# Performance work log

Hardware: AMD Instinct MI355X
Metric: run time of the kernel (lower is better)

Reference implementation:

```python
import jax, jax.numpy as jnp
import numpy as np

B, S, HID = 2, 2048, 4096
NH, NKV, HD = 32, 8, 128
SLIDING_WINDOW = 1024
ROPE_THETA = 10000.0


def setup_inputs() -> dict:
    key = jax.random.key(0)
    ks = jax.random.split(key, 6)
    hidden_states = jax.random.normal(ks[0], (B, S, HID), dtype=jnp.float32)
    attention_mask = jnp.ones((B, S), dtype=jnp.int32)
    position_ids = jnp.broadcast_to(jnp.arange(S, dtype=jnp.int32)[None, :], (B, S))
    sc = 1.0 / np.sqrt(HID)
    q_w = jax.random.normal(ks[1], (HID, NH * HD), dtype=jnp.float32) * sc
    k_w = jax.random.normal(ks[2], (HID, NKV * HD), dtype=jnp.float32) * sc
    v_w = jax.random.normal(ks[3], (HID, NKV * HD), dtype=jnp.float32) * sc
    o_w = jax.random.normal(ks[4], (NH * HD, HID), dtype=jnp.float32) * sc
    return {"hidden_states": hidden_states, "attention_mask": attention_mask,
            "position_ids": position_ids, "q_w": q_w, "k_w": k_w, "v_w": v_w, "o_w": o_w}


def _rotate_half(x):
    return jnp.concatenate((-x[..., x.shape[-1] // 2:], x[..., : x.shape[-1] // 2]), axis=-1)


def _rope_sincos(position_ids):
    # inv_freq over even dims of head_dim; emb = concat(freqs, freqs)
    inv_freq = 1.0 / ROPE_THETA ** (jnp.arange(0, HD, 2, dtype=jnp.float32) / HD)
    freqs = position_ids.astype(jnp.float32)[..., None] * inv_freq  # [B,S,HD/2]
    emb = jnp.concatenate((freqs, freqs), axis=-1)                  # [B,S,HD]
    # broadcast over heads axis: [B,S,1,HD]
    return jnp.sin(emb)[:, :, None, :], jnp.cos(emb)[:, :, None, :]


def reference(hidden_states, attention_mask, position_ids, q_w, k_w, v_w, o_w):
    b, q_len, _ = hidden_states.shape
    n_rep = NH // NKV

    q = (hidden_states @ q_w).reshape(b, q_len, NH, HD)
    k = (hidden_states @ k_w).reshape(b, q_len, NKV, HD)
    v = (hidden_states @ v_w).reshape(b, q_len, NKV, HD)

    sin_pos, cos_pos = _rope_sincos(position_ids)
    q = q * cos_pos + _rotate_half(q) * sin_pos
    k = k * cos_pos + _rotate_half(k) * sin_pos

    # GQA: repeat kv heads (repeat_interleave along head axis)
    k = jnp.repeat(k, n_rep, axis=2)  # [B,S,NH,HD]
    v = jnp.repeat(v, n_rep, axis=2)

    # sliding-window causal mask: j <= i and j >= i - sliding_window
    i = jnp.arange(q_len)[:, None]
    j = jnp.arange(q_len)[None, :]
    band = (j <= i) & (j >= i - SLIDING_WINDOW)           # [Q,K]
    mask = band[None, None] & (attention_mask[:, None, None, :] > 0)  # [B,1,Q,K]

    bias = jnp.where(mask, 0.0, jnp.finfo(jnp.float32).min)

    scale = 1.0 / jnp.sqrt(jnp.asarray(HD, dtype=jnp.float32))
    scores = jnp.einsum('bqhd,bkhd->bhqk', q, k) * scale + bias
    attn_weights = jax.nn.softmax(scores, axis=-1)
    attn_out = jnp.einsum('bhqk,bkhd->bqhd', attn_weights, v)
    attn_out = attn_out.reshape(b, q_len, HID)
    return attn_out @ o_w
```

## Files before the change

kernel.cpp:

```cpp
#include <hip/hip_runtime.h>
#include <stdint.h>
#include <stddef.h>

typedef __bf16 bf16x8 __attribute__((ext_vector_type(8)));
typedef short short8 __attribute__((ext_vector_type(8)));
typedef float floatx4 __attribute__((ext_vector_type(4)));
typedef unsigned short ushort4v __attribute__((ext_vector_type(4)));

__device__ __forceinline__ unsigned short f2bf(float f){
  unsigned int u = __float_as_uint(f);
  u += 0x7fffu + ((u >> 16) & 1u);
  return (unsigned short)(u >> 16);
}
__device__ __forceinline__ float bf2f(unsigned short s){
  return __uint_as_float(((unsigned int)s) << 16);
}
__device__ __forceinline__ void gl2lds16(const void* g, void* l){
  __builtin_amdgcn_global_load_lds((const __attribute__((address_space(1))) void*)g,
                                   (__attribute__((address_space(3))) void*)l, 16, 0, 0);
}

__global__ __launch_bounds__(256) void conv_f32_bf16(const float* __restrict__ in,
                                                     unsigned short* __restrict__ out){
  int t = blockIdx.x * 256 + threadIdx.x;
  floatx4 v = *(const floatx4*)(in + (size_t)t * 4);
  ushort4v o;
#pragma unroll
  for (int j = 0; j < 4; ++j) o[j] = f2bf(v[j]);
  *(ushort4v*)(out + (size_t)t * 4) = o;
}

__global__ __launch_bounds__(256) void transpose_cvt(const float* __restrict__ in,
                                                     unsigned short* __restrict__ out,
                                                     int Kd, int Nd){
  __shared__ __align__(16) unsigned short tile[64 * 80];
  int n0 = blockIdx.x * 64, k0 = blockIdx.y * 64;
  int t = threadIdx.x;
#pragma unroll
  for (int it = 0; it < 2; ++it){
    int rr = (t >> 3) + it * 32;
    int cc = t & 7;
    const float* src = in + (size_t)(k0 + rr) * Nd + n0 + cc * 8;
    floatx4 a = *(const floatx4*)src;
    floatx4 b = *(const floatx4*)(src + 4);
    short8 s;
#pragma unroll
    for (int j = 0; j < 4; ++j){ s[j] = (short)f2bf(a[j]); s[j + 4] = (short)f2bf(b[j]); }
    *(short8*)&tile[rr * 80 + cc * 8] = s;
  }
  __syncthreads();
#pragma unroll
  for (int it = 0; it < 2; ++it){
    int nr = (t >> 3) + it * 32;
    int kc = t & 7;
    short8 v;
#pragma unroll
    for (int j = 0; j < 8; ++j) v[j] = (short)tile[(kc * 8 + j) * 80 + nr];
    *(short8*)(out + (size_t)(n0 + nr) * Kd + k0 + kc * 8) = v;
  }
}

__global__ __launch_bounds__(256, 2) void gemm_bt(
    const unsigned short* __restrict__ A,
    const unsigned short* __restrict__ Wq,
    const unsigned short* __restrict__ Wk,
    const unsigned short* __restrict__ Wv,
    unsigned short* __restrict__ oQ,
    unsigned short* __restrict__ oK,
    unsigned short* __restrict__ oVt,
    float* __restrict__ oF, int f32out)
{
  __shared__ __align__(16) unsigned short As[128 * 64];
  __shared__ __align__(16) unsigned short Bs[128 * 64];
  const int tid = threadIdx.x;
  const int w = tid >> 6, lane = tid & 63, quad = lane >> 4, l15 = lane & 15;
  const int wm64 = (w >> 1) * 64, wn64 = (w & 1) * 64;
  const int m0 = blockIdx.y * 128;
  const int n0 = blockIdx.x * 128;

  const unsigned short* Wsrc;
  int nb, region;
  if (n0 < 4096)      { Wsrc = Wq; nb = n0;        region = 0; }
  else if (n0 < 5120) { Wsrc = Wk; nb = n0 - 4096; region = 1; }
  else                { Wsrc = Wv; nb = n0 - 5120; region = 2; }

  floatx4 acc[4][4];
#pragma unroll
  for (int i = 0; i < 4; ++i)
#pragma unroll
    for (int j = 0; j < 4; ++j) acc[i][j] = (floatx4){0.f, 0.f, 0.f, 0.f};

  const int rsub = lane >> 3, csub = lane & 7;

  for (int k0 = 0; k0 < 4096; k0 += 64){
#pragma unroll
    for (int i = 0; i < 4; ++i){
      int u = i * 4 + w;
      int r = u * 8 + rsub;
      gl2lds16(A    + ((size_t)(m0 + r) << 12) + k0 + ((csub ^ (r & 7)) << 3), (char*)As + u * 1024);
      gl2lds16(Wsrc + ((size_t)(nb + r) << 12) + k0 + ((csub ^ (r & 7)) << 3), (char*)Bs + u * 1024);
    }
    __syncthreads();
#pragma unroll
    for (int ks = 0; ks < 2; ++ks){
      bf16x8 af[4], bfr[4];
#pragma unroll
      for (int mt = 0; mt < 4; ++mt){
        int r = wm64 + mt * 16 + l15;
        int kc = ks * 4 + quad;
        af[mt] = *(const bf16x8*)&As[r * 64 + ((kc ^ (r & 7)) << 3)];
      }
#pragma unroll
      for (int nt = 0; nt < 4; ++nt){
        int r = wn64 + nt * 16 + l15;
        int kc = ks * 4 + quad;
        bfr[nt] = *(const bf16x8*)&Bs[r * 64 + ((kc ^ (r & 7)) << 3)];
      }
#pragma unroll
      for (int mt = 0; mt < 4; ++mt)
#pragma unroll
        for (int nt = 0; nt < 4; ++nt)
          acc[mt][nt] = __builtin_amdgcn_mfma_f32_16x16x32_bf16(af[mt], bfr[nt], acc[mt][nt], 0, 0, 0);
    }
    __syncthreads();
  }

  if (region == 0){
    if (f32out){
#pragma unroll
      for (int mt = 0; mt < 4; ++mt)
#pragma unroll
        for (int nt = 0; nt < 4; ++nt){
          int gn = n0 + wn64 + nt * 16 + l15;
#pragma unroll
          for (int rr = 0; rr < 4; ++rr){
            int gm = m0 + wm64 + mt * 16 + quad * 4 + rr;
            oF[((size_t)gm << 12) + gn] = acc[mt][nt][rr];
          }
        }
    } else {
#pragma unroll
      for (int mt = 0; mt < 4; ++mt)
#pragma unroll
        for (int nt = 0; nt < 4; ++nt){
          int gn = n0 + wn64 + nt * 16 + l15;
#pragma unroll
          for (int rr = 0; rr < 4; ++rr){
            int gm = m0 + wm64 + mt * 16 + quad * 4 + rr;
            oQ[((size_t)gm << 12) + gn] = f2bf(acc[mt][nt][rr]);
          }
        }
    }
  } else if (region == 1){
#pragma unroll
    for (int mt = 0; mt < 4; ++mt)
#pragma unroll
      for (int nt = 0; nt < 4; ++nt){
        int gn = n0 - 4096 + wn64 + nt * 16 + l15;
#pragma unroll
        for (int rr = 0; rr < 4; ++rr){
          int gm = m0 + wm64 + mt * 16 + quad * 4 + rr;
          oK[((size_t)gm << 10) + gn] = f2bf(acc[mt][nt][rr]);
        }
      }
  } else {
#pragma unroll
    for (int mt = 0; mt < 4; ++mt){
      int gm0 = m0 + wm64 + mt * 16 + quad * 4;
      int b = gm0 >> 11, s0 = gm0 & 2047;
#pragma unroll
      for (int nt = 0; nt < 4; ++nt){
        int dg = n0 - 5120 + wn64 + nt * 16 + l15;
        int kvh = dg >> 7, d = dg & 127;
        ushort4v pk;
#pragma unroll
        for (int rr = 0; rr < 4; ++rr) pk[rr] = f2bf(acc[mt][nt][rr]);
        *(ushort4v*)(oVt + (((size_t)(b * 8 + kvh) * 128 + d) * 2048 + s0)) = pk;
      }
    }
  }
}

__global__ void rope_apply_k(unsigned short* __restrict__ Qb, unsigned short* __restrict__ Kb,
                             const int* __restrict__ pos){
  int t = blockIdx.x * 256 + threadIdx.x;
  unsigned short* base;
  int row, ch;
  bool isq = (t < 1048576);
  if (isq){ row = t >> 8; int c = t & 255; base = Qb + ((size_t)row << 12) + (c >> 3) * 128; ch = c & 7; }
  else { int t2 = t - 1048576; row = t2 >> 6; int c = t2 & 63; base = Kb + ((size_t)row << 10) + (c >> 3) * 128; ch = c & 7; }
  float p = (float)pos[row];
  const float qs = 0.08838834764831845f * 1.44269504088896340736f;
  float sc_out = isq ? qs : 1.0f;
  int d0 = ch * 8;
  short8 x0 = *(short8*)(base + d0);
  short8 x1 = *(short8*)(base + d0 + 64);
  short8 y0, y1;
#pragma unroll
  for (int j = 0; j < 8; ++j){
    float ang = p * exp2f(-(float)(d0 + j) * 0.20762050593045952f);
    float sn = sinf(ang), cs = cosf(ang);
    float a  = bf2f((unsigned short)x0[j]);
    float bb = bf2f((unsigned short)x1[j]);
    y0[j] = (short)f2bf((a * cs - bb * sn) * sc_out);
    y1[j] = (short)f2bf((bb * cs + a * sn) * sc_out);
  }
  *(short8*)(base + d0)      = y0;
  *(short8*)(base + d0 + 64) = y1;
}

__global__ __launch_bounds__(256, 4) void flash_swa(
    const unsigned short* __restrict__ Q,
    const unsigned short* __restrict__ K,
    const unsigned short* __restrict__ Vt,
    const int* __restrict__ amask,
    unsigned short* __restrict__ attn)
{
  __shared__ __align__(16) unsigned short Kl[64 * 128];
  __shared__ __align__(16) unsigned short Vl[128 * 64];
  __shared__ __align__(16) unsigned short Pl[4 * 16 * 64];
  const int qt = blockIdx.x, h = blockIdx.y, b = blockIdx.z;
  const int kv = h >> 2;
  const int tid = threadIdx.x, w = tid >> 6, lane = tid & 63, quad = lane >> 4, l15 = lane & 15;
  const int q0 = qt * 64;

  bf16x8 qf[4];
  {
    const unsigned short* qbase = Q + (((size_t)(b * 2048 + q0 + w * 16 + l15)) << 12) + h * 128;
#pragma unroll
    for (int ks = 0; ks < 4; ++ks) qf[ks] = *(const bf16x8*)(qbase + ks * 32 + quad * 8);
  }
  floatx4 acco[8];
#pragma unroll
  for (int i = 0; i < 8; ++i) acco[i] = (floatx4){0.f, 0.f, 0.f, 0.f};
  float m_i[4] = {-1e30f, -1e30f, -1e30f, -1e30f};
  float l_i[4] = {0.f, 0.f, 0.f, 0.f};

  const int ts = (qt >= 16) ? (qt - 16) : 0;
  for (int jt = ts; jt <= qt; ++jt){
    const int k0 = jt * 64;
#pragma unroll
    for (int i = 0; i < 4; ++i){
      int u = i * 4 + w;
      int r = u * 4 + (lane >> 4);
      int c = lane & 15;
      gl2lds16(K + (((size_t)(b * 2048 + k0 + r)) << 10) + kv * 128 + ((c ^ (r & 15)) << 3),
               (char*)Kl + u * 1024);
    }
#pragma unroll
    for (int i = 0; i < 4; ++i){
      int u = i * 4 + w;
      int d = u * 8 + (lane >> 3);
      int c = lane & 7;
      gl2lds16(Vt + ((size_t)(b * 8 + kv) * 128 + d) * 2048 + k0 + ((c ^ (d & 7)) << 3),
               (char*)Vl + u * 1024);
    }
    int mkl = amask[b * 2048 + k0 + lane];
    bool allv = (__ballot(mkl > 0) == ~0ull);
    __syncthreads();

    floatx4 accs[4];
#pragma unroll
    for (int i = 0; i < 4; ++i) accs[i] = (floatx4){0.f, 0.f, 0.f, 0.f};
#pragma unroll
    for (int ks = 0; ks < 4; ++ks)
#pragma unroll
      for (int nt = 0; nt < 4; ++nt){
        int r = nt * 16 + l15;
        int kc = ks * 4 + quad;
        bf16x8 kf = *(const bf16x8*)&Kl[r * 128 + ((kc ^ (r & 15)) << 3)];
        accs[nt] = __builtin_amdgcn_mfma_f32_16x16x32_bf16(qf[ks], kf, accs[nt], 0, 0, 0);
      }

    bool slow = (jt == qt) || ((qt - jt) == 16) || (!allv);
    if (slow){
#pragma unroll
      for (int nt = 0; nt < 4; ++nt){
        int j = k0 + nt * 16 + l15;
        int mk = amask[b * 2048 + j];
#pragma unroll
        for (int rr = 0; rr < 4; ++rr){
          int irow = q0 + w * 16 + quad * 4 + rr;
          bool valid = (j <= irow) && (j >= irow - 1024) && (mk > 0);
          accs[nt][rr] = valid ? accs[nt][rr] : -1e30f;
        }
      }
    }

    float vmax[4]; float need = 0.f;
#pragma unroll
    for (int rr = 0; rr < 4; ++rr){
      float v = fmaxf(fmaxf(accs[0][rr], accs[1][rr]), fmaxf(accs[2][rr], accs[3][rr]));
#pragma unroll
      for (int d_ = 1; d_ < 16; d_ <<= 1) v = fmaxf(v, __shfl_xor(v, d_));
      vmax[rr] = v;
      need = fmaxf(need, v - m_i[rr]);
    }
    if (!__all(need <= 8.0f)){
#pragma unroll
      for (int rr = 0; rr < 4; ++rr){
        float mnew = fmaxf(m_i[rr], vmax[rr]);
        float alpha = exp2f(m_i[rr] - mnew);
        m_i[rr] = mnew;
        l_i[rr] *= alpha;
#pragma unroll
        for (int n2 = 0; n2 < 8; ++n2) acco[n2][rr] *= alpha;
      }
    }
#pragma unroll
    for (int rr = 0; rr < 4; ++rr){
      float rs = 0.f;
#pragma unroll
      for (int nt = 0; nt < 4; ++nt){
        float p = exp2f(accs[nt][rr] - m_i[rr]);
        accs[nt][rr] = p;
        rs += p;
      }
#pragma unroll
      for (int d_ = 1; d_ < 16; d_ <<= 1) rs += __shfl_xor(rs, d_);
      l_i[rr] += rs;
    }
#pragma unroll
    for (int nt = 0; nt < 4; ++nt)
#pragma unroll
      for (int rr = 0; rr < 4; ++rr){
        int row = quad * 4 + rr;
        Pl[w * 1024 + row * 64 + ((nt * 16 + l15) ^ ((row & 7) << 3))] = f2bf(accs[nt][rr]);
      }
#pragma unroll
    for (int ks2 = 0; ks2 < 2; ++ks2){
      bf16x8 pf = *(const bf16x8*)&Pl[w * 1024 + l15 * 64 + ((ks2 * 32 + quad * 8) ^ ((l15 & 7) << 3))];
#pragma unroll
      for (int n2 = 0; n2 < 8; ++n2){
        int d = n2 * 16 + l15;
        int sc = ks2 * 4 + quad;
        bf16x8 vf = *(const bf16x8*)&Vl[d * 64 + ((sc ^ (d & 7)) << 3)];
        acco[n2] = __builtin_amdgcn_mfma_f32_16x16x32_bf16(pf, vf, acco[n2], 0, 0, 0);
      }
    }
    __syncthreads();
  }

  float inv[4];
#pragma unroll
  for (int rr = 0; rr < 4; ++rr) inv[rr] = 1.f / l_i[rr];
#pragma unroll
  for (int n2 = 0; n2 < 8; ++n2)
#pragma unroll
    for (int rr = 0; rr < 4; ++rr){
      size_t off = (((size_t)(b * 2048 + q0 + w * 16 + quad * 4 + rr)) << 12) + h * 128 + n2 * 16 + l15;
      attn[off] = f2bf(acco[n2][rr] * inv[rr]);
    }
}

extern "C" void kernel_launch(void* const* d_in, const int* in_sizes, int n_in,
                              void* d_out, int out_size, void* d_ws, size_t ws_size,
                              hipStream_t stream){
  const float* hidden = (const float*)d_in[0];
  const int* amask = (const int*)d_in[1];
  const int* pos   = (const int*)d_in[2];
  const float* qw = (const float*)d_in[3];
  const float* kw = (const float*)d_in[4];
  const float* vw = (const float*)d_in[5];
  const float* ow = (const float*)d_in[6];

  char* ws = (char*)d_ws;
  unsigned short* hb   = (unsigned short*)(ws + 0);
  unsigned short* qt   = (unsigned short*)(ws + 33554432);
  unsigned short* kt   = (unsigned short*)(ws + 67108864);
  unsigned short* vtw  = (unsigned short*)(ws + 75497472);
  unsigned short* Qb   = (unsigned short*)(ws + 83886080);
  unsigned short* Kb   = (unsigned short*)(ws + 117440512);
  unsigned short* Vtb  = (unsigned short*)(ws + 125829120);
  unsigned short* ot   = hb;
  unsigned short* attn = qt;
  float* outp = (float*)d_out;

  hipLaunchKernelGGL(conv_f32_bf16, dim3(16384), dim3(256), 0, stream, hidden, hb);
  hipLaunchKernelGGL(transpose_cvt, dim3(64, 64), dim3(256), 0, stream, qw, qt, 4096, 4096);
  hipLaunchKernelGGL(transpose_cvt, dim3(16, 64), dim3(256), 0, stream, kw, kt, 4096, 1024);
  hipLaunchKernelGGL(transpose_cvt, dim3(16, 64), dim3(256), 0, stream, vw, vtw, 4096, 1024);
  hipLaunchKernelGGL(gemm_bt, dim3(48, 32), dim3(256), 0, stream,
                     hb, qt, kt, vtw, Qb, Kb, Vtb, (float*)nullptr, 0);
  hipLaunchKernelGGL(transpose_cvt, dim3(64, 64), dim3(256), 0, stream, ow, ot, 4096, 4096);
  hipLaunchKernelGGL(rope_apply_k, dim3(5120), dim3(256), 0, stream, Qb, Kb, pos);
  hipLaunchKernelGGL(flash_swa, dim3(32, 32, 2), dim3(256), 0, stream, Qb, Kb, Vtb, amask, attn);
  hipLaunchKernelGGL(gemm_bt, dim3(32, 32), dim3(256), 0, stream,
                     attn, ot, ot, ot, nullptr, nullptr, nullptr, outp, 1);
}
```

Before: 774.4 us.

## Double-buffer K/V tiles in sliding-window flash attention and raise MFMA priority

Splits the K and V shared-memory tiles into two buffers so the next key/value tile is fetched with global-to-LDS loads while the current tile is being computed on. This hides load latency behind the score and PV matrix multiplies, and drops the synchronisation that used to sit before each tile's compute. The attention-mask validity check now runs once per block over the whole sequence row instead of once per tile. MFMA sections are wrapped in s_setprio raises. In exchange, LDS use per block roughly doubles and the occupancy hint drops from 4 to 2 blocks, which reduces latency hiding across waves.

New measurement: 764.1 us. Within noise of the previous version (-1.3%).

```diff
diff --git a/kernel.cpp b/kernel.cpp
--- a/kernel.cpp
+++ b/kernel.cpp
@@ -209,21 +209,32 @@
   *(short8*)(base + d0 + 64) = y1;
 }
 
-__global__ __launch_bounds__(256, 4) void flash_swa(
+__global__ __launch_bounds__(256, 2) void flash_swa(
     const unsigned short* __restrict__ Q,
     const unsigned short* __restrict__ K,
     const unsigned short* __restrict__ Vt,
     const int* __restrict__ amask,
     unsigned short* __restrict__ attn)
 {
-  __shared__ __align__(16) unsigned short Kl[64 * 128];
-  __shared__ __align__(16) unsigned short Vl[128 * 64];
+  __shared__ __align__(16) unsigned short Kl[2][64 * 128];
+  __shared__ __align__(16) unsigned short Vl[2][128 * 64];
   __shared__ __align__(16) unsigned short Pl[4 * 16 * 64];
   const int qt = blockIdx.x, h = blockIdx.y, b = blockIdx.z;
   const int kv = h >> 2;
   const int tid = threadIdx.x, w = tid >> 6, lane = tid & 63, quad = lane >> 4, l15 = lane & 15;
   const int q0 = qt * 64;
 
+  bool anybad = false;
+  {
+    const int* ap = amask + b * 2048 + lane * 32;
+#pragma unroll
+    for (int i = 0; i < 8; ++i){
+      int4 mv = *(const int4*)(ap + i * 4);
+      anybad |= (mv.x <= 0) | (mv.y <= 0) | (mv.z <= 0) | (mv.w <= 0);
+    }
+  }
+  const bool allv = (__ballot(anybad) == 0ull);
+
   bf16x8 qf[4];
   {
     const unsigned short* qbase = Q + (((size_t)(b * 2048 + q0 + w * 16 + l15)) << 12) + h * 128;
@@ -237,40 +248,53 @@
   float l_i[4] = {0.f, 0.f, 0.f, 0.f};
 
   const int ts = (qt >= 16) ? (qt - 16) : 0;
+
+#define STAGE_KV(JT, BUF)                                                                  \
+  {                                                                                        \
+    const int k0s = (JT) * 64;                                                             \
+    _Pragma("unroll")                                                                      \
+    for (int i_ = 0; i_ < 4; ++i_){                                                        \
+      int u_ = i_ * 4 + w;                                                                 \
+      int r_ = u_ * 4 + (lane >> 4);                                                       \
+      int c_ = lane & 15;                                                                  \
+      gl2lds16(K + (((size_t)(b * 2048 + k0s + r_)) << 10) + kv * 128 + ((c_ ^ (r_ & 15)) << 3), \
+               (char*)Kl[BUF] + u_ * 1024);                                                \
+    }                                                                                      \
+    _Pragma("unroll")                                                                      \
+    for (int i_ = 0; i_ < 4; ++i_){                                                        \
+      int u_ = i_ * 4 + w;                                                                 \
+      int d_ = u_ * 8 + (lane >> 3);                                                       \
+      int c_ = lane & 7;                                                                   \
+      gl2lds16(Vt + ((size_t)(b * 8 + kv) * 128 + d_) * 2048 + k0s + ((c_ ^ (d_ & 7)) << 3), \
+               (char*)Vl[BUF] + u_ * 1024);                                                \
+    }                                                                                      \
+  }
+
+  STAGE_KV(ts, 0);
+  __syncthreads();
+
+  int cur = 0;
   for (int jt = ts; jt <= qt; ++jt){
     const int k0 = jt * 64;
-#pragma unroll
-    for (int i = 0; i < 4; ++i){
-      int u = i * 4 + w;
-      int r = u * 4 + (lane >> 4);
-      int c = lane & 15;
-      gl2lds16(K + (((size_t)(b * 2048 + k0 + r)) << 10) + kv * 128 + ((c ^ (r & 15)) << 3),
-               (char*)Kl + u * 1024);
-    }
-#pragma unroll
-    for (int i = 0; i < 4; ++i){
-      int u = i * 4 + w;
-      int d = u * 8 + (lane >> 3);
-      int c = lane & 7;
-      gl2lds16(Vt + ((size_t)(b * 8 + kv) * 128 + d) * 2048 + k0 + ((c ^ (d & 7)) << 3),
-               (char*)Vl + u * 1024);
-    }
-    int mkl = amask[b * 2048 + k0 + lane];
-    bool allv = (__ballot(mkl > 0) == ~0ull);
-    __syncthreads();
+    if (jt < qt) STAGE_KV(jt + 1, cur ^ 1);
+
+    const unsigned short* Klc = Kl[cur];
+    const unsigned short* Vlc = Vl[cur];
 
     floatx4 accs[4];
 #pragma unroll
     for (int i = 0; i < 4; ++i) accs[i] = (floatx4){0.f, 0.f, 0.f, 0.f};
+    __builtin_amdgcn_s_setprio(1);
 #pragma unroll
     for (int ks = 0; ks < 4; ++ks)
 #pragma unroll
       for (int nt = 0; nt < 4; ++nt){
         int r = nt * 16 + l15;
         int kc = ks * 4 + quad;
-        bf16x8 kf = *(const bf16x8*)&Kl[r * 128 + ((kc ^ (r & 15)) << 3)];
+        bf16x8 kf = *(const bf16x8*)&Klc[r * 128 + ((kc ^ (r & 15)) << 3)];
         accs[nt] = __builtin_amdgcn_mfma_f32_16x16x32_bf16(qf[ks], kf, accs[nt], 0, 0, 0);
       }
+    __builtin_amdgcn_s_setprio(0);
 
     bool slow = (jt == qt) || ((qt - jt) == 16) || (!allv);
     if (slow){
@@ -327,6 +351,7 @@
         int row = quad * 4 + rr;
         Pl[w * 1024 + row * 64 + ((nt * 16 + l15) ^ ((row & 7) << 3))] = f2bf(accs[nt][rr]);
       }
+    __builtin_amdgcn_s_setprio(1);
 #pragma unroll
     for (int ks2 = 0; ks2 < 2; ++ks2){
       bf16x8 pf = *(const bf16x8*)&Pl[w * 1024 + l15 * 64 + ((ks2 * 32 + quad * 8) ^ ((l15 & 7) << 3))];
@@ -334,12 +359,15 @@
       for (int n2 = 0; n2 < 8; ++n2){
         int d = n2 * 16 + l15;
         int sc = ks2 * 4 + quad;
-        bf16x8 vf = *(const bf16x8*)&Vl[d * 64 + ((sc ^ (d & 7)) << 3)];
+        bf16x8 vf = *(const bf16x8*)&Vlc[d * 64 + ((sc ^ (d & 7)) << 3)];
         acco[n2] = __builtin_amdgcn_mfma_f32_16x16x32_bf16(pf, vf, acco[n2], 0, 0, 0);
       }
     }
+    __builtin_amdgcn_s_setprio(0);
     __syncthreads();
-  }
+    cur ^= 1;
+  }
+#undef STAGE_KV
 
   float inv[4];
 #pragma unroll
```
